# Kernel tuning notes

Hardware: AMD Instinct MI355X
Metric: run time of the kernel (lower is better)

## Reference

```python
import jax, jax.numpy as jnp
import numpy as np

B, HW, ENC = 64, 14, 2048
L, V, E, D, A = 20, 10000, 512, 512, 512
T = L - 1  # max decode length (one caption forced to length L)


def setup_inputs() -> dict:
    key = jax.random.key(0)
    ks = jax.random.split(key, 16)

    def p(k, shape, s=0.02):
        return jax.random.normal(k, shape, jnp.float32) * s

    cl = jax.random.randint(ks[2], (B,), 5, L + 1).at[0].set(L)
    return {
        "encoder_out": jax.random.normal(ks[0], (B, HW, HW, ENC), jnp.float32),
        "encoded_captions": jax.random.randint(ks[1], (B, L), 0, V),
        "caption_lengths": cl[:, None].astype(jnp.int32),
        "emb": jax.random.uniform(ks[3], (V, E), jnp.float32, -0.1, 0.1),
        "W_ih": p(ks[4], (4 * D, E + ENC)), "b_ih": jnp.zeros((4 * D,), jnp.float32),
        "W_hh": p(ks[5], (4 * D, D)), "b_hh": jnp.zeros((4 * D,), jnp.float32),
        "W_init_h": p(ks[6], (D, ENC)), "b_init_h": jnp.zeros((D,), jnp.float32),
        "W_init_c": p(ks[7], (D, ENC)), "b_init_c": jnp.zeros((D,), jnp.float32),
        "W_fbeta": p(ks[8], (ENC, D)), "b_fbeta": jnp.zeros((ENC,), jnp.float32),
        "W_fc": jax.random.uniform(ks[9], (V, D), jnp.float32, -0.1, 0.1), "b_fc": jnp.zeros((V,), jnp.float32),
        "W_enc_att": p(ks[10], (A, ENC)), "b_enc_att": jnp.zeros((A,), jnp.float32),
        "W_dec_att": p(ks[11], (A, D)), "b_dec_att": jnp.zeros((A,), jnp.float32),
        "W_full_att": p(ks[12], (1, A)), "b_full_att": jnp.zeros((1,), jnp.float32),
    }


def _decode(encoder_out, encoded_captions, caption_lengths, emb,
            W_ih, b_ih, W_hh, b_hh, W_init_h, b_init_h, W_init_c, b_init_c,
            W_fbeta, b_fbeta, W_fc, b_fc, W_enc_att, b_enc_att,
            W_dec_att, b_dec_att, W_full_att, b_full_att):
    b = encoder_out.shape[0]
    enc = encoder_out.reshape(b, -1, encoder_out.shape[-1])  # [B, P, ENC]
    cl = caption_lengths[:, 0]
    sort_ind = jnp.argsort(-cl)  # descending by caption length
    cl = cl[sort_ind]
    enc = enc[sort_ind]
    caps = encoded_captions[sort_ind]
    decode_lengths = cl - 1  # per-sample number of decode steps

    mean_enc = jnp.mean(enc, axis=1)  # [B, ENC]
    h0 = mean_enc @ W_init_h.T + b_init_h
    c0 = mean_enc @ W_init_c.T + b_init_c

    embeddings = emb[caps]  # [B, L, E]
    # encoder-side attention projection is h-independent: precompute once
    att1 = jnp.einsum('bpe,ae->bpa', enc, W_enc_att) + b_enc_att  # [B, P, A]

    xs_emb = jnp.swapaxes(embeddings[:, :T], 0, 1)  # [T, B, E]
    masks = decode_lengths[None, :] > jnp.arange(T)[:, None]  # [T, B]
    # Note: torch slices h[:batch_size_t]; since batch is length-sorted descending,
    # masking inactive rows (freeze state, zero outputs) computes identical values.

    def step(carry, xs):
        h, c = carry
        emb_t, mask = xs
        # Bahdanau soft attention
        att2 = h @ W_dec_att.T + b_dec_att  # [B, A]
        e = jnp.einsum('bpa,a->bp', jnp.tanh(att1 + att2[:, None, :]), W_full_att[0]) + b_full_att[0]
        alpha = jax.nn.softmax(e, axis=1)  # [B, P]
        awe = jnp.einsum('bp,bpe->be', alpha, enc)  # [B, ENC]
        gate = jax.nn.sigmoid(h @ W_fbeta.T + b_fbeta)
        x = jnp.concatenate([emb_t, gate * awe], axis=1)  # [B, E+ENC]
        # LSTMCell (torch gate order: i, f, g, o)
        gates = x @ W_ih.T + b_ih + h @ W_hh.T + b_hh
        i, f, g, o = jnp.split(gates, 4, axis=1)
        c_new = jax.nn.sigmoid(f) * c + jax.nn.sigmoid(i) * jnp.tanh(g)
        h_new = jax.nn.sigmoid(o) * jnp.tanh(c_new)
        preds = h_new @ W_fc.T + b_fc  # dropout = identity in eval
        m = mask[:, None]
        h = jnp.where(m, h_new, h)
        c = jnp.where(m, c_new, c)
        return (h, c), (jnp.where(m, preds, 0.0), jnp.where(m, alpha, 0.0))

    (_, _), (preds, alphas) = jax.lax.scan(step, (h0, c0), (xs_emb, masks))
    predictions = jnp.swapaxes(preds, 0, 1)  # [B, T, V]
    alphas = jnp.swapaxes(alphas, 0, 1)      # [B, T, P]
    return predictions, caps, alphas, sort_ind


def reference(encoder_out, encoded_captions, caption_lengths, emb,
              W_ih, b_ih, W_hh, b_hh, W_init_h, b_init_h, W_init_c, b_init_c,
              W_fbeta, b_fbeta, W_fc, b_fc, W_enc_att, b_enc_att,
              W_dec_att, b_dec_att, W_full_att, b_full_att):
    return _decode(encoder_out, encoded_captions, caption_lengths, emb,
                   W_ih, b_ih, W_hh, b_hh, W_init_h, b_init_h, W_init_c, b_init_c,
                   W_fbeta, b_fbeta, W_fc, b_fc, W_enc_att, b_enc_att,
                   W_dec_att, b_dec_att, W_full_att, b_full_att)
```

## Files before the change

### kernel.cpp

```cpp
#include <hip/hip_runtime.h>
#include <math.h>

#define Bb 64
#define Pp 196
#define ENCd 2048
#define Lc 20
#define Tt 19
#define Vv 10000
#define Ee 512
#define Dd 512
#define Aa 512
#define K2 2560
#define KG 3072
#define G4 2048

#define OUT_PRED 0ll
#define OUT_CAPS 12160000ll
#define OUT_ALPH 12161280ll
#define OUT_SIND 12399616ll

typedef unsigned short ushort_t;
typedef __attribute__((ext_vector_type(8))) short short8;
typedef __attribute__((ext_vector_type(4))) float f32x4;

#define MFMA16 __builtin_amdgcn_mfma_f32_16x16x32_bf16

__device__ __forceinline__ float b2f(ushort_t u) {
    union { unsigned int i; float f; } x; x.i = ((unsigned int)u) << 16; return x.f;
}
__device__ __forceinline__ ushort_t f2b(float f) {
    union { float f; unsigned int i; } x; x.f = f;
    unsigned int r = x.i + 0x7fffu + ((x.i >> 16) & 1u);
    return (ushort_t)(r >> 16);
}
__device__ __forceinline__ float fsig(float x) { return 1.0f / (1.0f + __expf(-x)); }
__device__ __forceinline__ float ftanh(float x) {
    x = fminf(fmaxf(x, -15.0f), 15.0f);
    float e = __expf(2.0f * x);
    return (e - 1.0f) / (e + 1.0f);
}

__global__ void k_sort(const int* __restrict__ cap_len, const int* __restrict__ caps_in,
                       float* __restrict__ out, int* __restrict__ sind,
                       int* __restrict__ dlen, int* __restrict__ caps_s) {
    __shared__ int cls[Bb];
    int i = threadIdx.x;
    int cl = cap_len[i];
    cls[i] = cl;
    __syncthreads();
    int rank = 0;
    for (int j = 0; j < Bb; ++j) {
        int cj = cls[j];
        rank += (cj > cl) || (cj == cl && j < i);
    }
    sind[rank] = i;
    dlen[rank] = cl - 1;
    out[OUT_SIND + rank] = (float)i;
    for (int l = 0; l < Lc; ++l) {
        int v = caps_in[i * Lc + l];
        caps_s[rank * Lc + l] = v;
        out[OUT_CAPS + rank * Lc + l] = (float)v;
    }
}

__device__ __forceinline__ void cvtseg(const float* __restrict__ src, ushort_t* __restrict__ dst,
                                       int cols, int stride, int off, int bid0, long long quads) {
    long long qid = (long long)bid0 * 256 + threadIdx.x;
    if (qid >= quads) return;
    int c4pr = cols >> 2;
    int r = (int)(qid / c4pr), c4 = (int)(qid % c4pr) << 2;
    float4 v = *(const float4*)&src[(size_t)r * cols + c4];
    ushort4 o; o.x = f2b(v.x); o.y = f2b(v.y); o.z = f2b(v.z); o.w = f2b(v.w);
    *(ushort4*)&dst[(size_t)r * stride + off + c4] = o;
}

__global__ void k_cvtall(const float* Wdec, const float* Wfb, const float* Wih,
                         const float* Whh, const float* Wfc, const float* Wenc_f,
                         const float* Wih0, const float* Wic0,
                         ushort_t* W_ag, ushort_t* W_cat, ushort_t* W_fcb,
                         ushort_t* W_enc, ushort_t* W_hcb) {
    int b = blockIdx.x;
    if      (b < 256)   cvtseg(Wdec,  W_ag,               512,  512,  0,    b,         65536);
    else if (b < 1280)  cvtseg(Wfb,   W_ag + 512 * 512,   512,  512,  0,    b - 256,   262144);
    else if (b < 6400)  cvtseg(Wih,   W_cat,              2560, 3072, 0,    b - 1280,  1310720);
    else if (b < 7424)  cvtseg(Whh,   W_cat,              512,  3072, 2560, b - 6400,  262144);
    else if (b < 12424) cvtseg(Wfc,   W_fcb,              512,  512,  0,    b - 7424,  1280000);
    else if (b < 13448) cvtseg(Wenc_f,W_enc,              2048, 2048, 0,    b - 12424, 262144);
    else if (b < 14472) cvtseg(Wih0,  W_hcb,              2048, 2048, 0,    b - 13448, 262144);
    else                cvtseg(Wic0,  W_hcb + 512 * 2048, 2048, 2048, 0,    b - 14472, 262144);
}

__global__ void k_bias(const float* b_dec, const float* b_fb, const float* b_ihp,
                       const float* b_hhp, const float* b_h, const float* b_c,
                       float* b_ag, float* bsum, float* b_hc) {
    int id = blockIdx.x * 256 + threadIdx.x;
    if (id < 512) b_ag[id] = b_dec[id];
    else if (id < 2560) b_ag[id] = b_fb[id - 512];
    if (id < 2048) bsum[id] = b_ihp[id] + b_hhp[id];
    if (id < 512) b_hc[id] = b_h[id];
    else if (id < 1024) b_hc[id] = b_c[id - 512];
}

__global__ void __launch_bounds__(256) k_enccvt(const float* __restrict__ enc,
                                                const int* __restrict__ sind,
                                                ushort_t* __restrict__ enc_bf) {
    int r = blockIdx.x;
    int b = r / Pp;
    size_t srow = (size_t)sind[b] * Pp + (r - b * Pp);
    int e8 = threadIdx.x * 8;
    const float* s = enc + srow * ENCd + e8;
    float4 v0 = *(const float4*)s;
    float4 v1 = *(const float4*)(s + 4);
    short8 o;
    o[0] = (short)f2b(v0.x); o[1] = (short)f2b(v0.y); o[2] = (short)f2b(v0.z); o[3] = (short)f2b(v0.w);
    o[4] = (short)f2b(v1.x); o[5] = (short)f2b(v1.y); o[6] = (short)f2b(v1.z); o[7] = (short)f2b(v1.w);
    *(short8*)&enc_bf[(size_t)r * ENCd + e8] = o;
}

__global__ void __launch_bounds__(1024) k_meanenc(const ushort_t* __restrict__ enc_bf,
                                                  ushort_t* __restrict__ mean_bf) {
    int b = blockIdx.x;
    int lane = threadIdx.x & 63, w = threadIdx.x >> 6;
    int cg = w & 3, pg = w >> 2;
    int lc = cg * 512 + lane * 8;
    __shared__ float red[4][2048];
    float acc[8] = {};
    for (int p = pg; p < Pp; p += 4) {
        short8 v = *(const short8*)&enc_bf[((size_t)b * Pp + p) * ENCd + lc];
        #pragma unroll
        for (int j = 0; j < 8; ++j) acc[j] += b2f((ushort_t)v[j]);
    }
    #pragma unroll
    for (int j = 0; j < 8; ++j) red[pg][lc + j] = acc[j];
    __syncthreads();
    int tid = threadIdx.x;
    float2 s = {0.f, 0.f};
    #pragma unroll
    for (int g = 0; g < 4; ++g) {
        float2 v = *(const float2*)&red[g][tid * 2];
        s.x += v.x; s.y += v.y;
    }
    ushort2 o; o.x = f2b(s.x * (1.0f / Pp)); o.y = f2b(s.y * (1.0f / Pp));
    *(ushort2*)&mean_bf[(size_t)b * ENCd + tid * 2] = o;
}

__global__ void __launch_bounds__(256) k_att1(const ushort_t* __restrict__ enc_bf,
                                              const ushort_t* __restrict__ Wenc,
                                              const float* __restrict__ benc,
                                              ushort_t* __restrict__ att1) {
    __shared__ ushort_t As[128 * 64];
    __shared__ ushort_t Bs[128 * 64];
    int tid = threadIdx.x;
    int lane = tid & 63, w = tid >> 6;
    int wr = w >> 1, wc = w & 1;
    int m0 = blockIdx.y * 128, n0 = blockIdx.x * 128;
    int r16 = lane & 15;
    f32x4 acc[4][4];
    #pragma unroll
    for (int mf = 0; mf < 4; ++mf)
        #pragma unroll
        for (int nf = 0; nf < 4; ++nf) acc[mf][nf] = (f32x4){0.f, 0.f, 0.f, 0.f};

    int lrow = lane >> 3;
    int lslot = lane & 7;
    for (int k0 = 0; k0 < ENCd; k0 += 64) {
        __syncthreads();
        #pragma unroll
        for (int c = 0; c < 4; ++c) {
            int row = c * 32 + w * 8 + lrow;
            int kg = lslot ^ (row & 7);
            const ushort_t* asrc = enc_bf + (size_t)(m0 + row) * ENCd + k0 + kg * 8;
            const ushort_t* bsrc = Wenc   + (size_t)(n0 + row) * ENCd + k0 + kg * 8;
            __builtin_amdgcn_global_load_lds(
                (const __attribute__((address_space(1))) void*)asrc,
                (__attribute__((address_space(3))) void*)&As[(c * 32 + w * 8) * 64], 16, 0, 0);
            __builtin_amdgcn_global_load_lds(
                (const __attribute__((address_space(1))) void*)bsrc,
                (__attribute__((address_space(3))) void*)&Bs[(c * 32 + w * 8) * 64], 16, 0, 0);
        }
        __syncthreads();
        #pragma unroll
        for (int ks = 0; ks < 2; ++ks) {
            int sl = ks * 4 + (lane >> 4);
            short8 a[4], b[4];
            #pragma unroll
            for (int mf = 0; mf < 4; ++mf) {
                int row = wr * 64 + mf * 16 + r16;
                a[mf] = *(const short8*)&As[row * 64 + ((sl ^ (row & 7)) << 3)];
            }
            #pragma unroll
            for (int nf = 0; nf < 4; ++nf) {
                int row = wc * 64 + nf * 16 + r16;
                b[nf] = *(const short8*)&Bs[row * 64 + ((sl ^ (row & 7)) << 3)];
            }
            #pragma unroll
            for (int mf = 0; mf < 4; ++mf)
                #pragma unroll
                for (int nf = 0; nf < 4; ++nf)
                    acc[mf][nf] = MFMA16(a[mf], b[nf], acc[mf][nf], 0, 0, 0);
        }
    }
    int rj0 = (lane >> 4) << 2;
    #pragma unroll
    for (int mf = 0; mf < 4; ++mf)
        #pragma unroll
        for (int nf = 0; nf < 4; ++nf) {
            int col = n0 + wc * 64 + nf * 16 + r16;
            float bv = benc[col];
            #pragma unroll
            for (int j = 0; j < 4; ++j) {
                int row = m0 + wr * 64 + mf * 16 + rj0 + j;
                att1[(size_t)row * Aa + col] = f2b(acc[mf][nf][j] + bv);
            }
        }
}

__global__ void __launch_bounds__(256) k_h0c0(
        const ushort_t* __restrict__ A, const ushort_t* __restrict__ W,
        const float* __restrict__ bias, ushort_t* __restrict__ hout,
        float* __restrict__ cst) {
    int lane = threadIdx.x & 63, w = threadIdx.x >> 6;
    int r16 = lane & 15, kq = (lane >> 4) << 3;
    int ncol[4];
    #pragma unroll
    for (int tt = 0; tt < 4; ++tt) ncol[tt] = blockIdx.x * 64 + tt * 16 + r16;
    f32x4 acc[4][4];
    #pragma unroll
    for (int mt = 0; mt < 4; ++mt)
        #pragma unroll
        for (int tt = 0; tt < 4; ++tt) acc[mt][tt] = (f32x4){0.f, 0.f, 0.f, 0.f};
    for (int k0 = w * 512; k0 < w * 512 + 512; k0 += 32) {
        short8 a[4];
        #pragma unroll
        for (int mt = 0; mt < 4; ++mt)
            a[mt] = *(const short8*)(A + (size_t)(mt * 16 + r16) * ENCd + k0 + kq);
        #pragma unroll
        for (int tt = 0; tt < 4; ++tt) {
            short8 bw = *(const short8*)&W[(size_t)ncol[tt] * ENCd + k0 + kq];
            #pragma unroll
            for (int mt = 0; mt < 4; ++mt)
                acc[mt][tt] = MFMA16(a[mt], bw, acc[mt][tt], 0, 0, 0);
        }
    }
    __shared__ float red[2][64][68];
    if (w >= 2) {
        float* row = &red[w - 2][lane][0];
        #pragma unroll
        for (int mt = 0; mt < 4; ++mt)
            #pragma unroll
            for (int tt = 0; tt < 4; ++tt) *(f32x4*)&row[(mt * 4 + tt) * 4] = acc[mt][tt];
    }
    __syncthreads();
    if (w < 2) {
        float* row = &red[w][lane][0];
        #pragma unroll
        for (int mt = 0; mt < 4; ++mt)
            #pragma unroll
            for (int tt = 0; tt < 4; ++tt) acc[mt][tt] += *(f32x4*)&row[(mt * 4 + tt) * 4];
    }
    __syncthreads();
    if (w == 1) {
        float* row = &red[0][lane][0];
        #pragma unroll
        for (int mt = 0; mt < 4; ++mt)
            #pragma unroll
            for (int tt = 0; tt < 4; ++tt) *(f32x4*)&row[(mt * 4 + tt) * 4] = acc[mt][tt];
    }
    __syncthreads();
    if (w != 0) return;
    {
        float* row = &red[0][lane][0];
        #pragma unroll
        for (int mt = 0; mt < 4; ++mt)
            #pragma unroll
            for (int tt = 0; tt < 4; ++tt) acc[mt][tt] += *(f32x4*)&row[(mt * 4 + tt) * 4];
    }
    int rj0 = (lane >> 4) << 2;
    #pragma unroll
    for (int mt = 0; mt < 4; ++mt)
        #pragma unroll
        for (int tt = 0; tt < 4; ++tt) {
            int col = ncol[tt];
            float bv = bias[col];
            #pragma unroll
            for (int j = 0; j < 4; ++j) {
                int row = mt * 16 + rj0 + j;
                float v = acc[mt][tt][j] + bv;
                if (col < 512) hout[row * Dd + col] = f2b(v);
                else           cst[row * Dd + (col - 512)] = v;
            }
        }
}

__global__ void __launch_bounds__(256) k_ag(
        const ushort_t* __restrict__ h, const ushort_t* __restrict__ W,
        const float* __restrict__ bias, float* __restrict__ of) {
    int lane = threadIdx.x & 63, w = threadIdx.x >> 6;
    int r16 = lane & 15, kq = (lane >> 4) << 3;
    int col = blockIdx.x * 16 + r16;
    f32x4 acc[4];
    #pragma unroll
    for (int mt = 0; mt < 4; ++mt) acc[mt] = (f32x4){0.f, 0.f, 0.f, 0.f};
    for (int k0 = w * 128; k0 < w * 128 + 128; k0 += 32) {
        short8 bw = *(const short8*)&W[(size_t)col * Dd + k0 + kq];
        #pragma unroll
        for (int mt = 0; mt < 4; ++mt) {
            short8 a = *(const short8*)(h + (size_t)(mt * 16 + r16) * Dd + k0 + kq);
            acc[mt] = MFMA16(a, bw, acc[mt], 0, 0, 0);
        }
    }
    __shared__ float red[2][64][20];
    if (w >= 2) {
        float* rr = &red[w - 2][lane][0];
        #pragma unroll
        for (int mt = 0; mt < 4; ++mt) *(f32x4*)&rr[mt * 4] = acc[mt];
    }
    __syncthreads();
    if (w < 2) {
        float* rr = &red[w][lane][0];
        #pragma unroll
        for (int mt = 0; mt < 4; ++mt) acc[mt] += *(f32x4*)&rr[mt * 4];
    }
    __syncthreads();
    if (w == 1) {
        float* rr = &red[0][lane][0];
        #pragma unroll
        for (int mt = 0; mt < 4; ++mt) *(f32x4*)&rr[mt * 4] = acc[mt];
    }
    __syncthreads();
    if (w != 0) return;
    {
        float* rr = &red[0][lane][0];
        #pragma unroll
        for (int mt = 0; mt < 4; ++mt) acc[mt] += *(f32x4*)&rr[mt * 4];
    }
    int rj0 = (lane >> 4) << 2;
    float bv = bias[col];
    #pragma unroll
    for (int mt = 0; mt < 4; ++mt)
        #pragma unroll
        for (int j = 0; j < 4; ++j) {
            int row = mt * 16 + rj0 + j;
            float v = acc[mt][j] + bv;
            of[(size_t)row * K2 + col] = (col >= 512) ? fsig(v) : v;
        }
}

__global__ void __launch_bounds__(1024) k_esmawe(
        const ushort_t* __restrict__ att1, const float* __restrict__ ag,
        const float* __restrict__ wfull, const float* __restrict__ bfull,
        const ushort_t* __restrict__ enc_bf,
        const float* __restrict__ emb, const int* __restrict__ caps_s,
        ushort_t* __restrict__ x2, float* __restrict__ out,
        const int* __restrict__ dlen, int t) {
    int b = blockIdx.x >> 2, ch = blockIdx.x & 3;
    int tid = threadIdx.x;
    int lane = tid & 63, wv = tid >> 6;
    __shared__ float att2f[512], wfl[512];
    __shared__ float e_sh[200], al_sh[200], sm[4];
    __shared__ float redA[16][512];
    if (tid < 512) att2f[tid] = ag[(size_t)b * K2 + tid];
    else           wfl[tid - 512] = wfull[tid - 512];
    __syncthreads();
    float a2[8], wf8[8];
    #pragma unroll
    for (int j = 0; j < 8; ++j) { a2[j] = att2f[lane * 8 + j]; wf8[j] = wfl[lane * 8 + j]; }
    float bf0 = bfull[0];
    for (int p0 = wv; p0 < Pp; p0 += 32) {
        int p1 = p0 + 16;
        bool has1 = p1 < Pp;
        short8 v0 = *(const short8*)&att1[((size_t)b * Pp + p0) * Aa + lane * 8];
        short8 v1 = has1 ? *(const short8*)&att1[((size_t)b * Pp + p1) * Aa + lane * 8] : v0;
        float s0 = 0.f, s1 = 0.f;
        #pragma unroll
        for (int j = 0; j < 8; ++j) {
            s0 += ftanh(b2f((ushort_t)v0[j]) + a2[j]) * wf8[j];
            s1 += ftanh(b2f((ushort_t)v1[j]) + a2[j]) * wf8[j];
        }
        #pragma unroll
        for (int o = 32; o; o >>= 1) {
            s0 += __shfl_xor(s0, o);
            s1 += __shfl_xor(s1, o);
        }
        if (lane == 0) {
            e_sh[p0] = s0 + bf0;
            if (has1) e_sh[p1] = s1 + bf0;
        }
    }
    __syncthreads();
    if (wv == 0) {
        float v0 = e_sh[lane];
        float v1 = e_sh[lane + 64];
        float v2 = e_sh[lane + 128];
        float v3 = (lane + 192 < Pp) ? e_sh[lane + 192] : -1e30f;
        float m = fmaxf(fmaxf(v0, v1), fmaxf(v2, v3));
        #pragma unroll
        for (int o = 32; o; o >>= 1) m = fmaxf(m, __shfl_xor(m, o));
        float ss = __expf(v0 - m) + __expf(v1 - m) + __expf(v2 - m) + __expf(v3 - m);
        #pragma unroll
        for (int o = 32; o; o >>= 1) ss += __shfl_xor(ss, o);
        if (lane == 0) { sm[0] = m; sm[1] = 1.0f / ss; }
    } else if (ch == 0 && tid >= 512 && tid < 768) {
        int q = tid - 512;
        float2 e2v = *(const float2*)&emb[(size_t)caps_s[b * Lc + t] * Ee + q * 2];
        ushort2 o2; o2.x = f2b(e2v.x); o2.y = f2b(e2v.y);
        *(ushort2*)&x2[(size_t)b * K2 + q * 2] = o2;
    }
    __syncthreads();
    float mx = sm[0], inv = sm[1];
    if (tid < Pp) {
        float al = __expf(e_sh[tid] - mx) * inv;
        al_sh[tid] = al;
        if (ch == 0)
            out[OUT_ALPH + ((long long)b * Tt + t) * Pp + tid] = (t < dlen[b]) ? al : 0.0f;
    }
    __syncthreads();
    {
        int cg = tid & 63, pg = tid >> 6;
        int c0 = cg * 8;
        float acc[8] = {};
        const ushort_t* ep = enc_bf + (size_t)b * Pp * ENCd + ch * 512 + c0;
        for (int p = pg; p < Pp; p += 16) {
            float a = al_sh[p];
            short8 vv = *(const short8*)(ep + (size_t)p * ENCd);
            #pragma unroll
            for (int j = 0; j < 8; ++j) acc[j] += a * b2f((ushort_t)vv[j]);
        }
        *(f32x4*)&redA[pg][c0]     = *(f32x4*)&acc[0];
        *(f32x4*)&redA[pg][c0 + 4] = *(f32x4*)&acc[4];
    }
    __syncthreads();
    if (tid < 512) {
        float s = 0.f;
        #pragma unroll
        for (int g = 0; g < 16; ++g) s += redA[g][tid];
        int col = ch * 512 + tid;
        float gte = ag[(size_t)b * K2 + 512 + col];
        x2[(size_t)b * K2 + Ee + col] = f2b(gte * s);
    }
}

__global__ void __launch_bounds__(512) k_gates(
        const ushort_t* __restrict__ x2, const ushort_t* __restrict__ hin,
        const ushort_t* __restrict__ Wcat, const float* __restrict__ bsum,
        ushort_t* __restrict__ hout, float* __restrict__ cst,
        const int* __restrict__ dlen, int t) {
    int lane = threadIdx.x & 63, w = threadIdx.x >> 6;
    int r16 = lane & 15, kq = (lane >> 4) << 3;
    int m0 = blockIdx.y * 16;
    int d0 = blockIdx.x * 16;
    int row = m0 + r16;
    f32x4 acc[4];
    #pragma unroll
    for (int tt = 0; tt < 4; ++tt) acc[tt] = (f32x4){0.f, 0.f, 0.f, 0.f};
    for (int k0 = w * 384; k0 < w * 384 + 384; k0 += 32) {
        const ushort_t* s = (k0 < K2) ? (x2 + (size_t)row * K2 + k0 + kq)
                                      : (hin + (size_t)row * Dd + (k0 - K2) + kq);
        short8 a = *(const short8*)s;
        #pragma unroll
        for (int tt = 0; tt < 4; ++tt) {
            short8 bw = *(const short8*)&Wcat[(size_t)(d0 + tt * 512 + r16) * KG + k0 + kq];
            acc[tt] = MFMA16(a, bw, acc[tt], 0, 0, 0);
        }
    }
    __shared__ float red[4][64][20];
    for (int s2 = 4; s2; s2 >>= 1) {
        if (w >= s2 && w < 2 * s2) {
            float* rr = &red[w - s2][lane][0];
            #pragma unroll
            for (int tt = 0; tt < 4; ++tt) *(f32x4*)&rr[tt * 4] = acc[tt];
        }
        __syncthreads();
        if (w < s2) {
            float* rr = &red[w][lane][0];
            #pragma unroll
            for (int tt = 0; tt < 4; ++tt) acc[tt] += *(f32x4*)&rr[tt * 4];
        }
        __syncthreads();
    }
    if (w != 0) return;
    int rj0 = (lane >> 4) << 2;
    int d = d0 + r16;
    #pragma unroll
    for (int j = 0; j < 4; ++j) {
        int rw = m0 + rj0 + j;
        ushort_t hb;
        if (t < dlen[rw]) {
            float gi = acc[0][j] + bsum[d];
            float gf = acc[1][j] + bsum[512 + d];
            float gg = acc[2][j] + bsum[1024 + d];
            float go = acc[3][j] + bsum[1536 + d];
            float cv = cst[rw * Dd + d];
            float cn = fsig(gf) * cv + fsig(gi) * ftanh(gg);
            cst[rw * Dd + d] = cn;
            hb = f2b(fsig(go) * ftanh(cn));
        } else {
            hb = hin[rw * Dd + d];
        }
        hout[rw * Dd + d] = hb;
    }
}

__global__ void __launch_bounds__(256) k_preds(
        const ushort_t* __restrict__ hball, const ushort_t* __restrict__ Wfc,
        const float* __restrict__ bfc, const int* __restrict__ dlen,
        float* __restrict__ out) {
    __shared__ float lds[4][16][84];
    int lane = threadIdx.x & 63, w = threadIdx.x >> 6;
    int r16 = lane & 15, kq = (lane >> 4) << 3, rj0 = (lane >> 4) << 2;
    int ts = blockIdx.y * 4 + w;
    if (ts >= Tt) return;
    int n0 = blockIdx.x * 80;
    f32x4 acc[4][5];
    #pragma unroll
    for (int mt = 0; mt < 4; ++mt)
        #pragma unroll
        for (int tt = 0; tt < 5; ++tt) acc[mt][tt] = (f32x4){0.f, 0.f, 0.f, 0.f};
    const ushort_t* ap = hball + (size_t)((ts + 1) * Bb + r16) * Dd + kq;
    for (int k0 = 0; k0 < Dd; k0 += 32) {
        short8 a[4];
        #pragma unroll
        for (int mt = 0; mt < 4; ++mt)
            a[mt] = *(const short8*)(ap + (size_t)(mt * 16) * Dd + k0);
        #pragma unroll
        for (int tt = 0; tt < 5; ++tt) {
            short8 bw = *(const short8*)&Wfc[(size_t)(n0 + tt * 16 + r16) * Dd + k0 + kq];
            #pragma unroll
            for (int mt = 0; mt < 4; ++mt)
                acc[mt][tt] = MFMA16(a[mt], bw, acc[mt][tt], 0, 0, 0);
        }
    }
    #pragma unroll
    for (int mt = 0; mt < 4; ++mt) {
        #pragma unroll
        for (int tt = 0; tt < 5; ++tt) {
            float bv = bfc[n0 + tt * 16 + r16];
            #pragma unroll
            for (int j = 0; j < 4; ++j)
                lds[w][rj0 + j][tt * 16 + r16] = acc[mt][tt][j] + bv;
        }
        asm volatile("s_waitcnt lgkmcnt(0)" ::: "memory");
        #pragma unroll
        for (int c = 0; c < 5; ++c) {
            int idx = c * 64 + lane;
            int row = idx / 20, c4 = idx % 20;
            int b = mt * 16 + row;
            f32x4 v = *(f32x4*)&lds[w][row][c4 * 4];
            if (ts >= dlen[b]) v = (f32x4){0.f, 0.f, 0.f, 0.f};
            __builtin_nontemporal_store(v,
                (f32x4*)&out[OUT_PRED + ((long long)b * Tt + ts) * Vv + n0 + c4 * 4]);
        }
        asm volatile("s_waitcnt vmcnt(0)" ::: "memory");
    }
}

extern "C" void kernel_launch(void* const* d_in, const int* in_sizes, int n_in,
                              void* d_out, int out_size, void* d_ws, size_t ws_size,
                              hipStream_t stream) {
    const float* encoder_out      = (const float*)d_in[0];
    const int*   encoded_captions = (const int*)d_in[1];
    const int*   caption_lengths  = (const int*)d_in[2];
    const float* emb       = (const float*)d_in[3];
    const float* W_ih      = (const float*)d_in[4];
    const float* b_ih      = (const float*)d_in[5];
    const float* W_hh      = (const float*)d_in[6];
    const float* b_hh      = (const float*)d_in[7];
    const float* W_init_h  = (const float*)d_in[8];
    const float* b_init_h  = (const float*)d_in[9];
    const float* W_init_c  = (const float*)d_in[10];
    const float* b_init_c  = (const float*)d_in[11];
    const float* W_fbeta   = (const float*)d_in[12];
    const float* b_fbeta   = (const float*)d_in[13];
    const float* W_fc      = (const float*)d_in[14];
    const float* b_fc      = (const float*)d_in[15];
    const float* W_enc_att = (const float*)d_in[16];
    const float* b_enc_att = (const float*)d_in[17];
    const float* W_dec_att = (const float*)d_in[18];
    const float* b_dec_att = (const float*)d_in[19];
    const float* W_full_att = (const float*)d_in[20];
    const float* b_full_att = (const float*)d_in[21];
    float* out = (float*)d_out;

    char* p = (char*)d_ws;
    auto alloc = [&](size_t bytes) { char* r = p; p += (bytes + 255) & ~255ull; return r; };
    int* sind   = (int*)alloc(64 * 4);
    int* dlen   = (int*)alloc(64 * 4);
    int* caps_s = (int*)alloc(Bb * Lc * 4);
    float* c_st  = (float*)alloc(Bb * Dd * 4);
    float* ag    = (float*)alloc((size_t)Bb * K2 * 4);
    float* b_ag  = (float*)alloc(K2 * 4);
    float* bsum  = (float*)alloc(G4 * 4);
    float* b_hc  = (float*)alloc(1024 * 4);
    ushort_t* mean_bf = (ushort_t*)alloc((size_t)Bb * ENCd * 2);
    ushort_t* hball   = (ushort_t*)alloc((size_t)(Tt + 1) * Bb * Dd * 2);
    ushort_t* x2      = (ushort_t*)alloc((size_t)Bb * K2 * 2);
    ushort_t* att1    = (ushort_t*)alloc((size_t)Bb * Pp * Aa * 2);
    ushort_t* W_enc   = (ushort_t*)alloc((size_t)Aa * ENCd * 2);
    ushort_t* W_ag    = (ushort_t*)alloc((size_t)K2 * Dd * 2);
    ushort_t* W_cat   = (ushort_t*)alloc((size_t)G4 * KG * 2);
    ushort_t* W_fcb   = (ushort_t*)alloc((size_t)Vv * Dd * 2);
    ushort_t* W_hcb   = (ushort_t*)alloc((size_t)1024 * ENCd * 2);
    ushort_t* enc_bf  = (ushort_t*)alloc((size_t)Bb * Pp * ENCd * 2);

    k_sort<<<1, 64, 0, stream>>>(caption_lengths, encoded_captions, out, sind, dlen, caps_s);
    k_cvtall<<<15496, 256, 0, stream>>>(W_dec_att, W_fbeta, W_ih, W_hh, W_fc, W_enc_att,
                                        W_init_h, W_init_c, W_ag, W_cat, W_fcb, W_enc, W_hcb);
    k_bias<<<10, 256, 0, stream>>>(b_dec_att, b_fbeta, b_ih, b_hh, b_init_h, b_init_c,
                                   b_ag, bsum, b_hc);
    k_enccvt<<<12544, 256, 0, stream>>>(encoder_out, sind, enc_bf);
    k_meanenc<<<64, 1024, 0, stream>>>(enc_bf, mean_bf);
    k_h0c0<<<16, 256, 0, stream>>>(mean_bf, W_hcb, b_hc, hball, c_st);
    k_att1<<<dim3(4, 98), 256, 0, stream>>>(enc_bf, W_enc, b_enc_att, att1);

    for (int t = 0; t < Tt; ++t) {
        const ushort_t* hcur = hball + (size_t)t * Bb * Dd;
        ushort_t* hnext = hball + (size_t)(t + 1) * Bb * Dd;
        k_ag<<<160, 256, 0, stream>>>(hcur, W_ag, b_ag, ag);
        k_esmawe<<<256, 1024, 0, stream>>>(att1, ag, W_full_att, b_full_att, enc_bf,
            emb, caps_s, x2, out, dlen, t);
        k_gates<<<dim3(32, 4), 512, 0, stream>>>(x2, hcur, W_cat, bsum, hnext, c_st, dlen, t);
    }
    k_preds<<<dim3(125, 5), 256, 0, stream>>>(hball, W_fcb, b_fc, dlen, out);
}
```

Measured before the change: 1.184 ms.

## Retile output projection as LDS-staged GEMM, remap att1 blocks, grid-stride enc convert

The final vocabulary projection is rewritten as a 128x128 LDS-tiled MFMA GEMM over the flattened (timestep, batch) rows. Operands are loaded through global_load_lds with an XOR swizzle, replacing the per-wave direct-global loads, so weight tiles get reused across more rows. The att1 GEMM and the new preds kernel use a 1D grid with a block-index remap that groups tiles per XCD for better L2 locality. The encoder conversion becomes a grid-stride loop with fewer blocks. Buffers are padded (an extra hball slab, W_fc padded to 10112 rows) so tiles can read past the real bounds. The padded W_fc rows may not be initialised, but those outputs are masked out.

Result: faster. 1.152 ms (-2.7%).

```diff
diff --git a/kernel.cpp b/kernel.cpp
--- a/kernel.cpp
+++ b/kernel.cpp
@@ -13,6 +13,7 @@
 #define K2 2560
 #define KG 3072
 #define G4 2048
+#define NPAD 10112
 
 #define OUT_PRED 0ll
 #define OUT_CAPS 12160000ll
@@ -104,17 +105,22 @@
 __global__ void __launch_bounds__(256) k_enccvt(const float* __restrict__ enc,
                                                 const int* __restrict__ sind,
                                                 ushort_t* __restrict__ enc_bf) {
-    int r = blockIdx.x;
-    int b = r / Pp;
-    size_t srow = (size_t)sind[b] * Pp + (r - b * Pp);
-    int e8 = threadIdx.x * 8;
-    const float* s = enc + srow * ENCd + e8;
-    float4 v0 = *(const float4*)s;
-    float4 v1 = *(const float4*)(s + 4);
-    short8 o;
-    o[0] = (short)f2b(v0.x); o[1] = (short)f2b(v0.y); o[2] = (short)f2b(v0.z); o[3] = (short)f2b(v0.w);
-    o[4] = (short)f2b(v1.x); o[5] = (short)f2b(v1.y); o[6] = (short)f2b(v1.z); o[7] = (short)f2b(v1.w);
-    *(short8*)&enc_bf[(size_t)r * ENCd + e8] = o;
+    const long long total8 = (long long)Bb * Pp * ENCd / 8;
+    for (long long u = (long long)blockIdx.x * 256 + threadIdx.x; u < total8;
+         u += (long long)gridDim.x * 256) {
+        long long flat = u * 8;
+        int r = (int)(flat >> 11);
+        int c8 = (int)(flat & 2047);
+        int b = r / Pp;
+        size_t srow = (size_t)sind[b] * Pp + (r - b * Pp);
+        const float* s = enc + srow * ENCd + c8;
+        float4 v0 = *(const float4*)s;
+        float4 v1 = *(const float4*)(s + 4);
+        short8 o;
+        o[0] = (short)f2b(v0.x); o[1] = (short)f2b(v0.y); o[2] = (short)f2b(v0.z); o[3] = (short)f2b(v0.w);
+        o[4] = (short)f2b(v1.x); o[5] = (short)f2b(v1.y); o[6] = (short)f2b(v1.z); o[7] = (short)f2b(v1.w);
+        *(short8*)&enc_bf[(size_t)r * ENCd + c8] = o;
+    }
 }
 
 __global__ void __launch_bounds__(1024) k_meanenc(const ushort_t* __restrict__ enc_bf,
@@ -153,7 +159,10 @@
     int tid = threadIdx.x;
     int lane = tid & 63, w = tid >> 6;
     int wr = w >> 1, wc = w & 1;
-    int m0 = blockIdx.y * 128, n0 = blockIdx.x * 128;
+    int d = blockIdx.x;
+    int lid = (d & 7) * 49 + (d >> 3);
+    int by = lid >> 2, bx = lid & 3;
+    int m0 = by * 128, n0 = bx * 128;
     int r16 = lane & 15;
     f32x4 acc[4][4];
     #pragma unroll
@@ -502,53 +511,90 @@
 }
 
 __global__ void __launch_bounds__(256) k_preds(
-        const ushort_t* __restrict__ hball, const ushort_t* __restrict__ Wfc,
+        const ushort_t* __restrict__ hA, const ushort_t* __restrict__ Wfc,
         const float* __restrict__ bfc, const int* __restrict__ dlen,
         float* __restrict__ out) {
-    __shared__ float lds[4][16][84];
-    int lane = threadIdx.x & 63, w = threadIdx.x >> 6;
-    int r16 = lane & 15, kq = (lane >> 4) << 3, rj0 = (lane >> 4) << 2;
-    int ts = blockIdx.y * 4 + w;
-    if (ts >= Tt) return;
-    int n0 = blockIdx.x * 80;
-    f32x4 acc[4][5];
-    #pragma unroll
-    for (int mt = 0; mt < 4; ++mt)
-        #pragma unroll
-        for (int tt = 0; tt < 5; ++tt) acc[mt][tt] = (f32x4){0.f, 0.f, 0.f, 0.f};
-    const ushort_t* ap = hball + (size_t)((ts + 1) * Bb + r16) * Dd + kq;
-    for (int k0 = 0; k0 < Dd; k0 += 32) {
-        short8 a[4];
-        #pragma unroll
-        for (int mt = 0; mt < 4; ++mt)
-            a[mt] = *(const short8*)(ap + (size_t)(mt * 16) * Dd + k0);
-        #pragma unroll
-        for (int tt = 0; tt < 5; ++tt) {
-            short8 bw = *(const short8*)&Wfc[(size_t)(n0 + tt * 16 + r16) * Dd + k0 + kq];
-            #pragma unroll
-            for (int mt = 0; mt < 4; ++mt)
-                acc[mt][tt] = MFMA16(a[mt], bw, acc[mt][tt], 0, 0, 0);
-        }
-    }
-    #pragma unroll
-    for (int mt = 0; mt < 4; ++mt) {
-        #pragma unroll
-        for (int tt = 0; tt < 5; ++tt) {
-            float bv = bfc[n0 + tt * 16 + r16];
+    __shared__ ushort_t As[128 * 64];
+    __shared__ ushort_t Bs[128 * 64];
+    __shared__ float wb[4][16][66];
+    int tid = threadIdx.x;
+    int lane = tid & 63, w = tid >> 6;
+    int wr = w >> 1, wc = w & 1;
+    int d = blockIdx.x;
+    int x = d & 7, k = d >> 3;
+    int lid = (x < 6 ? x * 99 : 594 + (x - 6) * 98) + k;
+    int bx = lid / 10, by = lid % 10;
+    int m0 = by * 128, n0 = bx * 128;
+    int r16 = lane & 15;
+    f32x4 acc[4][4];
+    #pragma unroll
+    for (int mf = 0; mf < 4; ++mf)
+        #pragma unroll
+        for (int nf = 0; nf < 4; ++nf) acc[mf][nf] = (f32x4){0.f, 0.f, 0.f, 0.f};
+
+    int lrow = lane >> 3;
+    int lslot = lane & 7;
+    for (int k0 = 0; k0 < Dd; k0 += 64) {
+        __syncthreads();
+        #pragma unroll
+        for (int c = 0; c < 4; ++c) {
+            int row = c * 32 + w * 8 + lrow;
+            int kg = lslot ^ (row & 7);
+            const ushort_t* asrc = hA  + (size_t)(m0 + row) * Dd + k0 + kg * 8;
+            const ushort_t* bsrc = Wfc + (size_t)(n0 + row) * Dd + k0 + kg * 8;
+            __builtin_amdgcn_global_load_lds(
+                (const __attribute__((address_space(1))) void*)asrc,
+                (__attribute__((address_space(3))) void*)&As[(c * 32 + w * 8) * 64], 16, 0, 0);
+            __builtin_amdgcn_global_load_lds(
+                (const __attribute__((address_space(1))) void*)bsrc,
+                (__attribute__((address_space(3))) void*)&Bs[(c * 32 + w * 8) * 64], 16, 0, 0);
+        }
+        __syncthreads();
+        #pragma unroll
+        for (int ks = 0; ks < 2; ++ks) {
+            int sl = ks * 4 + (lane >> 4);
+            short8 a[4], b[4];
+            #pragma unroll
+            for (int mf = 0; mf < 4; ++mf) {
+                int row = wr * 64 + mf * 16 + r16;
+                a[mf] = *(const short8*)&As[row * 64 + ((sl ^ (row & 7)) << 3)];
+            }
+            #pragma unroll
+            for (int nf = 0; nf < 4; ++nf) {
+                int row = wc * 64 + nf * 16 + r16;
+                b[nf] = *(const short8*)&Bs[row * 64 + ((sl ^ (row & 7)) << 3)];
+            }
+            #pragma unroll
+            for (int mf = 0; mf < 4; ++mf)
+                #pragma unroll
+                for (int nf = 0; nf < 4; ++nf)
+                    acc[mf][nf] = MFMA16(a[mf], b[nf], acc[mf][nf], 0, 0, 0);
+        }
+    }
+    int rj0 = (lane >> 4) << 2;
+    #pragma unroll
+    for (int mf = 0; mf < 4; ++mf) {
+        #pragma unroll
+        for (int nf = 0; nf < 4; ++nf) {
+            float bv = bfc[n0 + wc * 64 + nf * 16 + r16];
             #pragma unroll
             for (int j = 0; j < 4; ++j)
-                lds[w][rj0 + j][tt * 16 + r16] = acc[mt][tt][j] + bv;
+                wb[w][rj0 + j][nf * 16 + r16] = acc[mf][nf][j] + bv;
         }
         asm volatile("s_waitcnt lgkmcnt(0)" ::: "memory");
         #pragma unroll
-        for (int c = 0; c < 5; ++c) {
+        for (int c = 0; c < 4; ++c) {
             int idx = c * 64 + lane;
-            int row = idx / 20, c4 = idx % 20;
-            int b = mt * 16 + row;
-            f32x4 v = *(f32x4*)&lds[w][row][c4 * 4];
-            if (ts >= dlen[b]) v = (f32x4){0.f, 0.f, 0.f, 0.f};
-            __builtin_nontemporal_store(v,
-                (f32x4*)&out[OUT_PRED + ((long long)b * Tt + ts) * Vv + n0 + c4 * 4]);
+            int row16 = idx >> 4, c4 = idx & 15;
+            int grow = m0 + wr * 64 + mf * 16 + row16;
+            int gcol = n0 + wc * 64 + c4 * 4;
+            if (grow < 1216 && gcol < Vv) {
+                int ts = grow >> 6, b = grow & 63;
+                f32x4 v = *(f32x4*)&wb[w][row16][c4 * 4];
+                if (ts >= dlen[b]) v = (f32x4){0.f, 0.f, 0.f, 0.f};
+                __builtin_nontemporal_store(v,
+                    (f32x4*)&out[OUT_PRED + ((long long)b * Tt + ts) * Vv + gcol]);
+            }
         }
         asm volatile("s_waitcnt vmcnt(0)" ::: "memory");
     }
@@ -592,13 +638,13 @@
     float* bsum  = (float*)alloc(G4 * 4);
     float* b_hc  = (float*)alloc(1024 * 4);
     ushort_t* mean_bf = (ushort_t*)alloc((size_t)Bb * ENCd * 2);
-    ushort_t* hball   = (ushort_t*)alloc((size_t)(Tt + 1) * Bb * Dd * 2);
+    ushort_t* hball   = (ushort_t*)alloc((size_t)(Tt + 2) * Bb * Dd * 2);
     ushort_t* x2      = (ushort_t*)alloc((size_t)Bb * K2 * 2);
     ushort_t* att1    = (ushort_t*)alloc((size_t)Bb * Pp * Aa * 2);
     ushort_t* W_enc   = (ushort_t*)alloc((size_t)Aa * ENCd * 2);
     ushort_t* W_ag    = (ushort_t*)alloc((size_t)K2 * Dd * 2);
     ushort_t* W_cat   = (ushort_t*)alloc((size_t)G4 * KG * 2);
-    ushort_t* W_fcb   = (ushort_t*)alloc((size_t)Vv * Dd * 2);
+    ushort_t* W_fcb   = (ushort_t*)alloc((size_t)NPAD * Dd * 2);
     ushort_t* W_hcb   = (ushort_t*)alloc((size_t)1024 * ENCd * 2);
     ushort_t* enc_bf  = (ushort_t*)alloc((size_t)Bb * Pp * ENCd * 2);
 
@@ -607,10 +653,10 @@
                                         W_init_h, W_init_c, W_ag, W_cat, W_fcb, W_enc, W_hcb);
     k_bias<<<10, 256, 0, stream>>>(b_dec_att, b_fbeta, b_ih, b_hh, b_init_h, b_init_c,
                                    b_ag, bsum, b_hc);
-    k_enccvt<<<12544, 256, 0, stream>>>(encoder_out, sind, enc_bf);
+    k_enccvt<<<2048, 256, 0, stream>>>(encoder_out, sind, enc_bf);
     k_meanenc<<<64, 1024, 0, stream>>>(enc_bf, mean_bf);
     k_h0c0<<<16, 256, 0, stream>>>(mean_bf, W_hcb, b_hc, hball, c_st);
-    k_att1<<<dim3(4, 98), 256, 0, stream>>>(enc_bf, W_enc, b_enc_att, att1);
+    k_att1<<<392, 256, 0, stream>>>(enc_bf, W_enc, b_enc_att, att1);
 
     for (int t = 0; t < Tt; ++t) {
         const ushort_t* hcur = hball + (size_t)t * Bb * Dd;
@@ -620,5 +666,5 @@
             emb, caps_s, x2, out, dlen, t);
         k_gates<<<dim3(32, 4), 512, 0, stream>>>(x2, hcur, W_cat, bsum, hnext, c_st, dlen, t);
     }
-    k_preds<<<dim3(125, 5), 256, 0, stream>>>(hball, W_fcb, b_fc, dlen, out);
-}
+    k_preds<<<790, 256, 0, stream>>>(hball + (size_t)Bb * Dd, W_fcb, b_fc, dlen, out);
+}
```
